# Kernel optimization log

Hardware: AMD Instinct MI355X
Metric: run time of the kernel (lower is better)

Reference implementation:

```python
import jax, jax.numpy as jnp
import numpy as np

B, N, D, H = 4, 512, 64, 8
DK = D // H


def setup_inputs() -> dict:
    key = jax.random.key(0)
    ks = jax.random.split(key, 9)
    s = 0.05
    return {
        "n": jax.random.normal(ks[0], (B, N, D), jnp.float32),
        "e": jax.random.normal(ks[1], (B, N, N, D), jnp.float32),
        "Wq": jax.random.normal(ks[2], (D, D), jnp.float32) * s,
        "Wk": jax.random.normal(ks[3], (D, D), jnp.float32) * s,
        "Wv": jax.random.normal(ks[4], (D, D), jnp.float32) * s,
        "Wo": jax.random.normal(ks[5], (D, D), jnp.float32) * s,
        "Wg": jax.random.normal(ks[6], (D, H), jnp.float32) * s,
        "We": jax.random.normal(ks[7], (D, H), jnp.float32) * s,
        "Oe": jax.random.normal(ks[8], (H, D), jnp.float32) * s,
    }


def reference(n, e, Wq, Wk, Wv, Wo, Wg, We, Oe):
    b, nn_, d = n.shape
    # Q,K,V: (B,H,N,DK)
    Q = (n @ Wq).reshape(b, nn_, H, DK).transpose(0, 2, 1, 3)
    K = (n @ Wk).reshape(b, nn_, H, DK).transpose(0, 2, 1, 3)
    V = (n @ Wv).reshape(b, nn_, H, DK).transpose(0, 2, 1, 3)
    # Edge bias E and gate G: (B,H,N,N)
    Eb = jnp.einsum('bqmd,dh->bhqm', e, We)
    G = jax.nn.sigmoid(jnp.einsum('bqmd,dh->bhqm', e, Wg))
    dyn_centrality = jnp.log1p(G.sum(-1))  # (B,H,N)
    # Scaled, clamped attention scores with edge bias
    A = jnp.einsum('bhqd,bhmd->bhqm', Q, K) * (DK ** -0.5)
    A = jnp.clip(A, -5.0, 5.0)
    Ehat = A + Eb
    P = jax.nn.softmax(Ehat, axis=-1)
    Vo = jnp.einsum('bhqm,bhmd->bhqd', P, V)
    Vo = Vo * dyn_centrality[..., None]
    n_out = Vo.transpose(0, 2, 1, 3).reshape(b, nn_, d) @ Wo
    e_out = jnp.einsum('bhqm,hd->bqmd', Ehat, Oe)
    return n_out, e_out
```

## Files before the change

### kernel.cpp

```cpp
#include <hip/hip_runtime.h>
#include <math.h>

#define Bn 4
#define Nn 512
#define Dn 64
#define Hn 8
#define TR 64
#define NT (Nn / TR)
#define EW 68
#define PS 68
#define PART 80

__global__ __launch_bounds__(64) void qkv_kernel(
    const float* __restrict__ nin, const float* __restrict__ Wq,
    const float* __restrict__ Wk, const float* __restrict__ Wv,
    float* __restrict__ Qw, float* __restrict__ Kw, float* __restrict__ Vw)
{
    const int row = blockIdx.x;
    const int d = threadIdx.x;
    __shared__ float nrow[Dn];
    nrow[d] = nin[row * Dn + d];
    __syncthreads();
    float aq = 0.f, ak = 0.f, av = 0.f;
#pragma unroll
    for (int k = 0; k < Dn; ++k) {
        const float nv = nrow[k];
        aq = fmaf(nv, Wq[k * Dn + d], aq);
        ak = fmaf(nv, Wk[k * Dn + d], ak);
        av = fmaf(nv, Wv[k * Dn + d], av);
    }
    Qw[row * Dn + d] = aq;
    Kw[row * Dn + d] = ak;
    Vw[row * Dn + d] = av;
}

__global__ __launch_bounds__(256, 5) void stream_kernel(
    const float* __restrict__ e,
    const float* __restrict__ Qw, const float* __restrict__ Kw,
    const float* __restrict__ Vw,
    const float* __restrict__ WeG, const float* __restrict__ WgG,
    const float* __restrict__ OeG,
    float* __restrict__ eout, float* __restrict__ part)
{
    const int bid  = blockIdx.x;
    const int bq   = bid >> 3;
    const int tile = bid & 7;
    const int b    = bq >> 9;
    const int m0   = tile * TR;
    const int t    = threadIdx.x;
    const int w    = t >> 6;
    const int l    = t & 63;

    __shared__ float e_tile[TR * EW];
    __shared__ float ehat_s[Hn * PS];
    __shared__ float p_s[Hn * PS];
    __shared__ __align__(16) float we_s[Hn][Dn];
    __shared__ __align__(16) float wg_s[Hn][Dn];
    __shared__ __align__(16) float oe_s[Hn][Dn];
    __shared__ float accb[4][Dn];
    __shared__ float psb[4][Dn];
    __shared__ float gsb[4][Hn];

    float4 st[4];
    {
        const float4* ep = (const float4*)(e + ((size_t)bq * Nn + m0) * Dn);
#pragma unroll
        for (int j = 0; j < 4; ++j) st[j] = ep[j * 256 + t];
    }

    float a0, a1;
    {
        const float4* kp = (const float4*)(Kw + ((size_t)b * Nn + m0 + l) * Dn + w * 16);
        const float4 k0 = kp[0], k1 = kp[1], k2 = kp[2], k3 = kp[3];
        const float4* qp = (const float4*)(Qw + (size_t)bq * Dn + w * 16);
        const float4 q0 = qp[0], q1 = qp[1], q2 = qp[2], q3 = qp[3];
        const float qscale = 0.35355339059327373f;
        a0 = k0.x*q0.x + k0.y*q0.y + k0.z*q0.z + k0.w*q0.w
           + k1.x*q1.x + k1.y*q1.y + k1.z*q1.z + k1.w*q1.w;
        a1 = k2.x*q2.x + k2.y*q2.y + k2.z*q2.z + k2.w*q2.w
           + k3.x*q3.x + k3.y*q3.y + k3.z*q3.z + k3.w*q3.w;
        a0 = fminf(fmaxf(a0 * qscale, -5.f), 5.f);
        a1 = fminf(fmaxf(a1 * qscale, -5.f), 5.f);
    }

    for (int i = t; i < Dn * Hn; i += 256) {
        const int d = i >> 3, h = i & 7;
        we_s[h][d] = WeG[i];
        wg_s[h][d] = WgG[i];
        ((float*)oe_s)[i] = OeG[i];
    }

#pragma unroll
    for (int j = 0; j < 4; ++j) {
        const int c = j * 256 + t, r = c >> 4, cc = c & 15;
        *(float4*)&e_tile[r * EW + cc * 4] = st[j];
    }
    __syncthreads();

    float eb0 = 0.f, eb1 = 0.f, gg0 = 0.f, gg1 = 0.f;
    {
        const float4* we0 = (const float4*)we_s[2 * w];
        const float4* we1 = (const float4*)we_s[2 * w + 1];
        const float4* wg0 = (const float4*)wg_s[2 * w];
        const float4* wg1 = (const float4*)wg_s[2 * w + 1];
#pragma unroll
        for (int d4 = 0; d4 < 16; ++d4) {
            const float4 e4 = *(const float4*)&e_tile[l * EW + d4 * 4];
            const float4 A0 = we0[d4], A1 = we1[d4];
            const float4 G0 = wg0[d4], G1 = wg1[d4];
            eb0 = fmaf(e4.x, A0.x, fmaf(e4.y, A0.y, fmaf(e4.z, A0.z, fmaf(e4.w, A0.w, eb0))));
            eb1 = fmaf(e4.x, A1.x, fmaf(e4.y, A1.y, fmaf(e4.z, A1.z, fmaf(e4.w, A1.w, eb1))));
            gg0 = fmaf(e4.x, G0.x, fmaf(e4.y, G0.y, fmaf(e4.z, G0.z, fmaf(e4.w, G0.w, gg0))));
            gg1 = fmaf(e4.x, G1.x, fmaf(e4.y, G1.y, fmaf(e4.z, G1.z, fmaf(e4.w, G1.w, gg1))));
        }
    }

    {
        const float eh0 = a0 + eb0, eh1 = a1 + eb1;
        ehat_s[(2 * w) * PS + l]     = eh0;
        ehat_s[(2 * w + 1) * PS + l] = eh1;
        p_s[(2 * w) * PS + l]     = __expf(eh0);
        p_s[(2 * w + 1) * PS + l] = __expf(eh1);
        float g0 = 1.f / (1.f + __expf(-gg0));
        float g1 = 1.f / (1.f + __expf(-gg1));
#pragma unroll
        for (int off = 32; off > 0; off >>= 1) {
            g0 += __shfl_xor(g0, off, 64);
            g1 += __shfl_xor(g1, off, 64);
        }
        if (l == 0) { gsb[w][2 * w] = g0; gsb[w][2 * w + 1] = g1; }
    }
    __syncthreads();

    {
        float eh[Hn];
#pragma unroll
        for (int h = 0; h < Hn; ++h) eh[h] = ehat_s[h * PS + l];
#pragma unroll
        for (int j = 0; j < 4; ++j) {
            float4 o; o.x = o.y = o.z = o.w = 0.f;
#pragma unroll
            for (int h = 0; h < Hn; ++h) {
                const float4 w4 = *(const float4*)&oe_s[h][w * 16 + j * 4];
                o.x = fmaf(eh[h], w4.x, o.x);
                o.y = fmaf(eh[h], w4.y, o.y);
                o.z = fmaf(eh[h], w4.z, o.z);
                o.w = fmaf(eh[h], w4.w, o.w);
            }
            *(float4*)&e_tile[l * EW + w * 16 + j * 4] = o;
        }
    }
    __syncthreads();

    {
        float4* eo = (float4*)(eout + ((size_t)bq * Nn + m0) * Dn);
#pragma unroll
        for (int j = 0; j < 4; ++j) {
            const int c = j * 256 + t;
            eo[c] = *(const float4*)&e_tile[(c >> 4) * EW + (c & 15) * 4];
        }
    }

    {
        const int h = l >> 3;
        float acc = 0.f, ps = 0.f;
        const float* vrow = Vw + ((size_t)b * Nn + m0 + w * 16) * Dn;
#pragma unroll
        for (int i = 0; i < 16; ++i) {
            const float p = p_s[h * PS + w * 16 + i];
            ps += p;
            acc = fmaf(p, vrow[i * Dn + l], acc);
        }
        accb[w][l] = acc;
        psb[w][l]  = ps;
    }
    __syncthreads();

    if (w == 0) {
        const int h = l >> 3;
        const float O = accb[0][l] + accb[1][l] + accb[2][l] + accb[3][l];
        const float S = psb[0][l] + psb[1][l] + psb[2][l] + psb[3][l];
        float* pb = part + (size_t)bid * PART;
        pb[l] = O;
        if ((l & 7) == 0) pb[64 + h] = S;
        if (l < 8)        pb[72 + l] = gsb[l >> 1][l];
    }
}

__global__ __launch_bounds__(64) void reduce_kernel(
    const float* __restrict__ part, const float* __restrict__ WoG,
    float* __restrict__ nout)
{
    const int bq = blockIdx.x;
    const int l  = threadIdx.x;
    const int h  = l >> 3;
    const float* pb = part + (size_t)bq * NT * PART;
    float O = 0.f, S = 0.f, G = 0.f;
#pragma unroll
    for (int tl = 0; tl < NT; ++tl) {
        O += pb[tl * PART + l];
        S += pb[tl * PART + 64 + h];
        G += pb[tl * PART + 72 + h];
    }
    __shared__ float vo_s[Dn];
    vo_s[l] = (O / S) * log1pf(G);
    __syncthreads();
    float a = 0.f;
#pragma unroll
    for (int k = 0; k < Dn; ++k)
        a = fmaf(vo_s[k], WoG[k * Dn + l], a);
    nout[(size_t)bq * Dn + l] = a;
}

extern "C" void kernel_launch(void* const* d_in, const int* in_sizes, int n_in,
                              void* d_out, int out_size, void* d_ws, size_t ws_size,
                              hipStream_t stream)
{
    (void)in_sizes; (void)n_in; (void)out_size; (void)ws_size;
    const float* nin = (const float*)d_in[0];
    const float* e   = (const float*)d_in[1];
    const float* Wq  = (const float*)d_in[2];
    const float* Wk  = (const float*)d_in[3];
    const float* Wv  = (const float*)d_in[4];
    const float* Wo  = (const float*)d_in[5];
    const float* Wg  = (const float*)d_in[6];
    const float* We  = (const float*)d_in[7];
    const float* Oe  = (const float*)d_in[8];

    float* Qw   = (float*)d_ws;
    float* Kw   = Qw + Bn * Nn * Dn;
    float* Vw   = Kw + Bn * Nn * Dn;
    float* part = Vw + Bn * Nn * Dn;

    float* nout = (float*)d_out;
    float* eout = nout + Bn * Nn * Dn;

    qkv_kernel<<<Bn * Nn, 64, 0, stream>>>(nin, Wq, Wk, Wv, Qw, Kw, Vw);
    stream_kernel<<<Bn * Nn * NT, 256, 0, stream>>>(e, Qw, Kw, Vw, We, Wg, Oe,
                                                    eout, part);
    reduce_kernel<<<Bn * Nn, 64, 0, stream>>>(part, Wo, nout);
}
```

Before: 138.8 us.

## Swizzle edge tile, write e_out directly with nontemporal stores, drop p_s buffer

Replaces the padded edge tile with an XOR-swizzled unpadded layout to cut LDS use and avoid bank conflicts. The e_out projection is now computed per output float4 and written straight to global memory with nontemporal stores, which removes a staging pass through shared memory and one barrier. Softmax denominators come from wave shuffle reductions, and exp values are recomputed from ehat_s instead of being stored in a separate p_s buffer. Occupancy hint is raised to 6 blocks per CU; the cost is redundant exp and ehat reads.

```diff
diff --git a/kernel.cpp b/kernel.cpp
--- a/kernel.cpp
+++ b/kernel.cpp
@@ -7,9 +7,10 @@
 #define Hn 8
 #define TR 64
 #define NT (Nn / TR)
-#define EW 68
 #define PS 68
 #define PART 80
+
+typedef float f32x4 __attribute__((ext_vector_type(4)));
 
 __global__ __launch_bounds__(64) void qkv_kernel(
     const float* __restrict__ nin, const float* __restrict__ Wq,
@@ -34,7 +35,7 @@
     Vw[row * Dn + d] = av;
 }
 
-__global__ __launch_bounds__(256, 5) void stream_kernel(
+__global__ __launch_bounds__(256, 6) void stream_kernel(
     const float* __restrict__ e,
     const float* __restrict__ Qw, const float* __restrict__ Kw,
     const float* __restrict__ Vw,
@@ -51,15 +52,13 @@
     const int w    = t >> 6;
     const int l    = t & 63;
 
-    __shared__ float e_tile[TR * EW];
+    __shared__ float e_tile[TR * Dn];
     __shared__ float ehat_s[Hn * PS];
-    __shared__ float p_s[Hn * PS];
     __shared__ __align__(16) float we_s[Hn][Dn];
     __shared__ __align__(16) float wg_s[Hn][Dn];
     __shared__ __align__(16) float oe_s[Hn][Dn];
     __shared__ float accb[4][Dn];
-    __shared__ float psb[4][Dn];
-    __shared__ float gsb[4][Hn];
+    __shared__ float ssb[Hn], gsb[Hn];
 
     float4 st[4];
     {
@@ -92,8 +91,8 @@
 
 #pragma unroll
     for (int j = 0; j < 4; ++j) {
-        const int c = j * 256 + t, r = c >> 4, cc = c & 15;
-        *(float4*)&e_tile[r * EW + cc * 4] = st[j];
+        const int c = j * 256 + t, r = c >> 4, g = c & 15;
+        *(float4*)&e_tile[r * Dn + ((g ^ (r & 15)) << 2)] = st[j];
     }
     __syncthreads();
 
@@ -105,7 +104,7 @@
         const float4* wg1 = (const float4*)wg_s[2 * w + 1];
 #pragma unroll
         for (int d4 = 0; d4 < 16; ++d4) {
-            const float4 e4 = *(const float4*)&e_tile[l * EW + d4 * 4];
+            const float4 e4 = *(const float4*)&e_tile[l * Dn + (((d4 ^ (l & 15))) << 2)];
             const float4 A0 = we0[d4], A1 = we1[d4];
             const float4 G0 = wg0[d4], G1 = wg1[d4];
             eb0 = fmaf(e4.x, A0.x, fmaf(e4.y, A0.y, fmaf(e4.z, A0.z, fmaf(e4.w, A0.w, eb0))));
@@ -119,71 +118,60 @@
         const float eh0 = a0 + eb0, eh1 = a1 + eb1;
         ehat_s[(2 * w) * PS + l]     = eh0;
         ehat_s[(2 * w + 1) * PS + l] = eh1;
-        p_s[(2 * w) * PS + l]     = __expf(eh0);
-        p_s[(2 * w + 1) * PS + l] = __expf(eh1);
+        float p0 = __expf(eh0), p1 = __expf(eh1);
         float g0 = 1.f / (1.f + __expf(-gg0));
         float g1 = 1.f / (1.f + __expf(-gg1));
 #pragma unroll
         for (int off = 32; off > 0; off >>= 1) {
+            p0 += __shfl_xor(p0, off, 64);
+            p1 += __shfl_xor(p1, off, 64);
             g0 += __shfl_xor(g0, off, 64);
             g1 += __shfl_xor(g1, off, 64);
         }
-        if (l == 0) { gsb[w][2 * w] = g0; gsb[w][2 * w + 1] = g1; }
-    }
-    __syncthreads();
-
-    {
-        float eh[Hn];
-#pragma unroll
-        for (int h = 0; h < Hn; ++h) eh[h] = ehat_s[h * PS + l];
+        if (l == 0) {
+            ssb[2 * w] = p0; ssb[2 * w + 1] = p1;
+            gsb[2 * w] = g0; gsb[2 * w + 1] = g1;
+        }
+    }
+    __syncthreads();
+
+    {
+        float4* eo = (float4*)(eout + ((size_t)bq * Nn + m0) * Dn);
 #pragma unroll
         for (int j = 0; j < 4; ++j) {
-            float4 o; o.x = o.y = o.z = o.w = 0.f;
+            const int c = j * 256 + t, r = c >> 4, cc = c & 15;
+            f32x4 o = {0.f, 0.f, 0.f, 0.f};
 #pragma unroll
             for (int h = 0; h < Hn; ++h) {
-                const float4 w4 = *(const float4*)&oe_s[h][w * 16 + j * 4];
-                o.x = fmaf(eh[h], w4.x, o.x);
-                o.y = fmaf(eh[h], w4.y, o.y);
-                o.z = fmaf(eh[h], w4.z, o.z);
-                o.w = fmaf(eh[h], w4.w, o.w);
+                const float ehv = ehat_s[h * PS + r];
+                const float4 w4 = *(const float4*)&oe_s[h][cc * 4];
+                o.x = fmaf(ehv, w4.x, o.x);
+                o.y = fmaf(ehv, w4.y, o.y);
+                o.z = fmaf(ehv, w4.z, o.z);
+                o.w = fmaf(ehv, w4.w, o.w);
             }
-            *(float4*)&e_tile[l * EW + w * 16 + j * 4] = o;
-        }
-    }
-    __syncthreads();
-
-    {
-        float4* eo = (float4*)(eout + ((size_t)bq * Nn + m0) * Dn);
-#pragma unroll
-        for (int j = 0; j < 4; ++j) {
-            const int c = j * 256 + t;
-            eo[c] = *(const float4*)&e_tile[(c >> 4) * EW + (c & 15) * 4];
+            __builtin_nontemporal_store(o, (f32x4*)eo + c);
         }
     }
 
     {
         const int h = l >> 3;
-        float acc = 0.f, ps = 0.f;
+        float acc = 0.f;
         const float* vrow = Vw + ((size_t)b * Nn + m0 + w * 16) * Dn;
 #pragma unroll
         for (int i = 0; i < 16; ++i) {
-            const float p = p_s[h * PS + w * 16 + i];
-            ps += p;
+            const float p = __expf(ehat_s[h * PS + w * 16 + i]);
             acc = fmaf(p, vrow[i * Dn + l], acc);
         }
         accb[w][l] = acc;
-        psb[w][l]  = ps;
     }
     __syncthreads();
 
     if (w == 0) {
-        const int h = l >> 3;
         const float O = accb[0][l] + accb[1][l] + accb[2][l] + accb[3][l];
-        const float S = psb[0][l] + psb[1][l] + psb[2][l] + psb[3][l];
         float* pb = part + (size_t)bid * PART;
         pb[l] = O;
-        if ((l & 7) == 0) pb[64 + h] = S;
-        if (l < 8)        pb[72 + l] = gsb[l >> 1][l];
+        if (l < 8) { pb[64 + l] = ssb[l]; pb[72 + l] = gsb[l]; }
     }
 }
 
```

Result: faster. 130.5 us (-6.0%).

## Remap stream kernel threads to quarter-rows, dropping LDS edge tile staging

Applied to the files above, without the earlier changes.

Each thread now loads a 16-float slice of one edge row directly into registers and computes partial edge-bias and gate projections for all eight heads, combined via lane shuffles. This removes the shared-memory e tile, its store/load round trip and two block barriers, and writes e_out straight from registers. Gate sums are reduced through shared memory alongside softmax sums, and launch bounds raise the occupancy target. It costs more registers per thread and extra shuffle/select logic for redistributing attention scores.

```diff
diff --git a/kernel.cpp b/kernel.cpp
--- a/kernel.cpp
+++ b/kernel.cpp
@@ -7,7 +7,6 @@
 #define Hn 8
 #define TR 64
 #define NT (Nn / TR)
-#define EW 68
 #define PS 68
 #define PART 80
 
@@ -34,7 +33,7 @@
     Vw[row * Dn + d] = av;
 }
 
-__global__ __launch_bounds__(256, 5) void stream_kernel(
+__global__ __launch_bounds__(256, 6) void stream_kernel(
     const float* __restrict__ e,
     const float* __restrict__ Qw, const float* __restrict__ Kw,
     const float* __restrict__ Vw,
@@ -50,38 +49,29 @@
     const int t    = threadIdx.x;
     const int w    = t >> 6;
     const int l    = t & 63;
-
-    __shared__ float e_tile[TR * EW];
-    __shared__ float ehat_s[Hn * PS];
-    __shared__ float p_s[Hn * PS];
+    const int r    = l >> 2;
+    const int dq   = l & 3;
+    const int row  = w * 16 + r;
+    const int m    = m0 + row;
+
     __shared__ __align__(16) float we_s[Hn][Dn];
     __shared__ __align__(16) float wg_s[Hn][Dn];
     __shared__ __align__(16) float oe_s[Hn][Dn];
+    __shared__ float ps_s[Hn][PS];
+    __shared__ float gs_s[Hn][PS];
     __shared__ float accb[4][Dn];
-    __shared__ float psb[4][Dn];
+    __shared__ float smb[4][Hn];
     __shared__ float gsb[4][Hn];
 
-    float4 st[4];
-    {
-        const float4* ep = (const float4*)(e + ((size_t)bq * Nn + m0) * Dn);
-#pragma unroll
-        for (int j = 0; j < 4; ++j) st[j] = ep[j * 256 + t];
-    }
-
-    float a0, a1;
-    {
-        const float4* kp = (const float4*)(Kw + ((size_t)b * Nn + m0 + l) * Dn + w * 16);
-        const float4 k0 = kp[0], k1 = kp[1], k2 = kp[2], k3 = kp[3];
-        const float4* qp = (const float4*)(Qw + (size_t)bq * Dn + w * 16);
-        const float4 q0 = qp[0], q1 = qp[1], q2 = qp[2], q3 = qp[3];
-        const float qscale = 0.35355339059327373f;
-        a0 = k0.x*q0.x + k0.y*q0.y + k0.z*q0.z + k0.w*q0.w
-           + k1.x*q1.x + k1.y*q1.y + k1.z*q1.z + k1.w*q1.w;
-        a1 = k2.x*q2.x + k2.y*q2.y + k2.z*q2.z + k2.w*q2.w
-           + k3.x*q3.x + k3.y*q3.y + k3.z*q3.z + k3.w*q3.w;
-        a0 = fminf(fmaxf(a0 * qscale, -5.f), 5.f);
-        a1 = fminf(fmaxf(a1 * qscale, -5.f), 5.f);
-    }
+    const float4* ep = (const float4*)(e + ((size_t)bq * Nn + m) * Dn + dq * 16);
+    float4 ev[4];
+#pragma unroll
+    for (int j = 0; j < 4; ++j) ev[j] = ep[j];
+
+    const float4* kp = (const float4*)(Kw + ((size_t)b * Nn + m) * Dn + dq * 16);
+    const float4 k0 = kp[0], k1 = kp[1], k2 = kp[2], k3 = kp[3];
+    const float4* qp = (const float4*)(Qw + (size_t)bq * Dn + dq * 16);
+    const float4 q0 = qp[0], q1 = qp[1], q2 = qp[2], q3 = qp[3];
 
     for (int i = t; i < Dn * Hn; i += 256) {
         const int d = i >> 3, h = i & 7;
@@ -90,100 +80,108 @@
         ((float*)oe_s)[i] = OeG[i];
     }
 
+    const float qscale = 0.35355339059327373f;
+    float a0 = k0.x*q0.x + k0.y*q0.y + k0.z*q0.z + k0.w*q0.w
+             + k1.x*q1.x + k1.y*q1.y + k1.z*q1.z + k1.w*q1.w;
+    float a1 = k2.x*q2.x + k2.y*q2.y + k2.z*q2.z + k2.w*q2.w
+             + k3.x*q3.x + k3.y*q3.y + k3.z*q3.z + k3.w*q3.w;
+    a0 = fminf(fmaxf(a0 * qscale, -5.f), 5.f);
+    a1 = fminf(fmaxf(a1 * qscale, -5.f), 5.f);
+
+    __syncthreads();
+
+    float ebp[Hn], ggp[Hn];
+#pragma unroll
+    for (int h = 0; h < Hn; ++h) { ebp[h] = 0.f; ggp[h] = 0.f; }
 #pragma unroll
     for (int j = 0; j < 4; ++j) {
-        const int c = j * 256 + t, r = c >> 4, cc = c & 15;
-        *(float4*)&e_tile[r * EW + cc * 4] = st[j];
-    }
-    __syncthreads();
-
-    float eb0 = 0.f, eb1 = 0.f, gg0 = 0.f, gg1 = 0.f;
+        const float4 e4 = ev[j];
+#pragma unroll
+        for (int h = 0; h < Hn; ++h) {
+            const float4 wv = *(const float4*)&we_s[h][dq * 16 + j * 4];
+            const float4 gv = *(const float4*)&wg_s[h][dq * 16 + j * 4];
+            ebp[h] = fmaf(e4.x, wv.x, fmaf(e4.y, wv.y,
+                      fmaf(e4.z, wv.z, fmaf(e4.w, wv.w, ebp[h]))));
+            ggp[h] = fmaf(e4.x, gv.x, fmaf(e4.y, gv.y,
+                      fmaf(e4.z, gv.z, fmaf(e4.w, gv.w, ggp[h]))));
+        }
+    }
+
+#pragma unroll
+    for (int h = 0; h < Hn; ++h) {
+        ebp[h] += __shfl_xor(ebp[h], 1, 64);
+        ebp[h] += __shfl_xor(ebp[h], 2, 64);
+        ggp[h] += __shfl_xor(ggp[h], 1, 64);
+        ggp[h] += __shfl_xor(ggp[h], 2, 64);
+    }
+
+    const float n0 = __shfl_xor(a0, 1, 64);
+    const float n1 = __shfl_xor(a1, 1, 64);
+    const bool odd = dq & 1, hi = dq & 2;
+    const float h40 = odd ? n0 : a0, h41 = odd ? n1 : a1;
+    const float h42 = odd ? a0 : n0, h43 = odd ? a1 : n1;
+    const float g0 = __shfl_xor(h40, 2, 64), g1 = __shfl_xor(h41, 2, 64);
+    const float g2 = __shfl_xor(h42, 2, 64), g3 = __shfl_xor(h43, 2, 64);
+    float eh[Hn];
+    eh[0] = (hi ? g0 : h40) + ebp[0];
+    eh[1] = (hi ? g1 : h41) + ebp[1];
+    eh[2] = (hi ? g2 : h42) + ebp[2];
+    eh[3] = (hi ? g3 : h43) + ebp[3];
+    eh[4] = (hi ? h40 : g0) + ebp[4];
+    eh[5] = (hi ? h41 : g1) + ebp[5];
+    eh[6] = (hi ? h42 : g2) + ebp[6];
+    eh[7] = (hi ? h43 : g3) + ebp[7];
+
     {
-        const float4* we0 = (const float4*)we_s[2 * w];
-        const float4* we1 = (const float4*)we_s[2 * w + 1];
-        const float4* wg0 = (const float4*)wg_s[2 * w];
-        const float4* wg1 = (const float4*)wg_s[2 * w + 1];
-#pragma unroll
-        for (int d4 = 0; d4 < 16; ++d4) {
-            const float4 e4 = *(const float4*)&e_tile[l * EW + d4 * 4];
-            const float4 A0 = we0[d4], A1 = we1[d4];
-            const float4 G0 = wg0[d4], G1 = wg1[d4];
-            eb0 = fmaf(e4.x, A0.x, fmaf(e4.y, A0.y, fmaf(e4.z, A0.z, fmaf(e4.w, A0.w, eb0))));
-            eb1 = fmaf(e4.x, A1.x, fmaf(e4.y, A1.y, fmaf(e4.z, A1.z, fmaf(e4.w, A1.w, eb1))));
-            gg0 = fmaf(e4.x, G0.x, fmaf(e4.y, G0.y, fmaf(e4.z, G0.z, fmaf(e4.w, G0.w, gg0))));
-            gg1 = fmaf(e4.x, G1.x, fmaf(e4.y, G1.y, fmaf(e4.z, G1.z, fmaf(e4.w, G1.w, gg1))));
-        }
+        const float eo0 = hi ? (odd ? eh[6] : eh[4]) : (odd ? eh[2] : eh[0]);
+        const float eo1 = hi ? (odd ? eh[7] : eh[5]) : (odd ? eh[3] : eh[1]);
+        const float go0 = hi ? (odd ? ggp[6] : ggp[4]) : (odd ? ggp[2] : ggp[0]);
+        const float go1 = hi ? (odd ? ggp[7] : ggp[5]) : (odd ? ggp[3] : ggp[1]);
+        ps_s[2 * dq][row]     = __expf(eo0);
+        ps_s[2 * dq + 1][row] = __expf(eo1);
+        gs_s[2 * dq][row]     = 1.f / (1.f + __expf(-go0));
+        gs_s[2 * dq + 1][row] = 1.f / (1.f + __expf(-go1));
     }
 
     {
-        const float eh0 = a0 + eb0, eh1 = a1 + eb1;
-        ehat_s[(2 * w) * PS + l]     = eh0;
-        ehat_s[(2 * w + 1) * PS + l] = eh1;
-        p_s[(2 * w) * PS + l]     = __expf(eh0);
-        p_s[(2 * w + 1) * PS + l] = __expf(eh1);
-        float g0 = 1.f / (1.f + __expf(-gg0));
-        float g1 = 1.f / (1.f + __expf(-gg1));
-#pragma unroll
-        for (int off = 32; off > 0; off >>= 1) {
-            g0 += __shfl_xor(g0, off, 64);
-            g1 += __shfl_xor(g1, off, 64);
-        }
-        if (l == 0) { gsb[w][2 * w] = g0; gsb[w][2 * w + 1] = g1; }
-    }
-    __syncthreads();
-
-    {
-        float eh[Hn];
-#pragma unroll
-        for (int h = 0; h < Hn; ++h) eh[h] = ehat_s[h * PS + l];
+        float4* eo = (float4*)(eout + ((size_t)bq * Nn + m) * Dn + dq * 16);
 #pragma unroll
         for (int j = 0; j < 4; ++j) {
             float4 o; o.x = o.y = o.z = o.w = 0.f;
 #pragma unroll
             for (int h = 0; h < Hn; ++h) {
-                const float4 w4 = *(const float4*)&oe_s[h][w * 16 + j * 4];
+                const float4 w4 = *(const float4*)&oe_s[h][dq * 16 + j * 4];
                 o.x = fmaf(eh[h], w4.x, o.x);
                 o.y = fmaf(eh[h], w4.y, o.y);
                 o.z = fmaf(eh[h], w4.z, o.z);
                 o.w = fmaf(eh[h], w4.w, o.w);
             }
-            *(float4*)&e_tile[l * EW + w * 16 + j * 4] = o;
+            eo[j] = o;
         }
     }
-    __syncthreads();
-
-    {
-        float4* eo = (float4*)(eout + ((size_t)bq * Nn + m0) * Dn);
-#pragma unroll
-        for (int j = 0; j < 4; ++j) {
-            const int c = j * 256 + t;
-            eo[c] = *(const float4*)&e_tile[(c >> 4) * EW + (c & 15) * 4];
-        }
-    }
-
-    {
-        const int h = l >> 3;
-        float acc = 0.f, ps = 0.f;
-        const float* vrow = Vw + ((size_t)b * Nn + m0 + w * 16) * Dn;
-#pragma unroll
-        for (int i = 0; i < 16; ++i) {
-            const float p = p_s[h * PS + w * 16 + i];
-            ps += p;
-            acc = fmaf(p, vrow[i * Dn + l], acc);
-        }
-        accb[w][l] = acc;
-        psb[w][l]  = ps;
-    }
+
+    const int hc = l >> 3;
+    float sm = 0.f, gsum = 0.f, acc = 0.f;
+    const float* vb = Vw + ((size_t)b * Nn + m0 + w * 16) * Dn;
+#pragma unroll
+    for (int i = 0; i < 16; ++i) {
+        const float p = ps_s[hc][w * 16 + i];
+        sm += p;
+        gsum += gs_s[hc][w * 16 + i];
+        acc = fmaf(p, vb[i * Dn + l], acc);
+    }
+    accb[w][l] = acc;
+    if ((l & 7) == 0) { smb[w][hc] = sm; gsb[w][hc] = gsum; }
     __syncthreads();
 
     if (w == 0) {
-        const int h = l >> 3;
         const float O = accb[0][l] + accb[1][l] + accb[2][l] + accb[3][l];
-        const float S = psb[0][l] + psb[1][l] + psb[2][l] + psb[3][l];
         float* pb = part + (size_t)bid * PART;
         pb[l] = O;
-        if ((l & 7) == 0) pb[64 + h] = S;
-        if (l < 8)        pb[72 + l] = gsb[l >> 1][l];
+        if (l < 8) {
+            pb[64 + l] = smb[0][l] + smb[1][l] + smb[2][l] + smb[3][l];
+            pb[72 + l] = gsb[0][l] + gsb[1][l] + gsb[2][l] + gsb[3][l];
+        }
     }
 }
 
```

New measurement: 156.8 us. 1.13x slower.
